# Optimization experiments

Measured on AMD Instinct MI355X. Metric: run time of the kernel, lower is better.

Reference implementation:

```python
import jax, jax.numpy as jnp
import numpy as np
import math

N, C, T, V = 32, 64, 400, 27
S = 2            # num_subset
IC = 16          # inter_channels
EPS = 1e-5


def _spatial_pe(channels, num_node):
    # PositionalEncoding(domain='spatial'): pe[c, t, v] depends only on joint id v
    pos = jnp.arange(num_node, dtype=jnp.float32)                      # [V]
    div = jnp.exp(jnp.arange(0, channels, 2, dtype=jnp.float32)
                  * (-math.log(10000.0) / channels))                   # [C/2]
    ang = div[:, None] * pos[None, :]                                  # [C/2, V]
    pe = jnp.stack([jnp.sin(ang), jnp.cos(ang)], axis=1)               # [C/2, 2, V]
    return pe.reshape(channels, num_node)                              # [C, V]


def _conv1x1(x, w, b):
    # x: [N, Cin, T, V], w: [Cout, Cin]
    return jnp.einsum('nctv,oc->notv', x, w) + b[None, :, None, None]


def _bn(x, g, b, m, v):
    inv = g / jnp.sqrt(v + EPS)
    return x * inv[None, :, None, None] + (b - m * inv)[None, :, None, None]


def _leaky(x):
    return jnp.where(x >= 0, x, 0.1 * x)


def setup_inputs() -> dict:
    key = jax.random.key(0)
    ks = jax.random.split(key, 24)
    d = {}
    d['x'] = jax.random.normal(ks[0], (N, C, T, V), jnp.float32)
    d['w_in'] = jax.random.normal(ks[1], (2 * S * IC, C), jnp.float32) * 0.1
    d['b_in'] = jax.random.normal(ks[2], (2 * S * IC,), jnp.float32) * 0.05
    d['alphas'] = jnp.ones((1, S, 1, 1), jnp.float32)
    d['att0'] = jax.random.uniform(ks[3], (1, S, V, V), jnp.float32) / V
    d['w_outs'] = jax.random.normal(ks[4], (C, S * C), jnp.float32) * 0.08
    d['b_outs'] = jax.random.normal(ks[5], (C,), jnp.float32) * 0.05
    d['bn_outs_g'] = jax.random.uniform(ks[6], (C,), jnp.float32) + 0.5
    d['bn_outs_b'] = jax.random.normal(ks[7], (C,), jnp.float32) * 0.05
    d['bn_outs_m'] = jax.random.normal(ks[8], (C,), jnp.float32) * 0.1
    d['bn_outs_v'] = jax.random.uniform(ks[9], (C,), jnp.float32) + 0.5
    d['w_ff'] = jax.random.normal(ks[10], (C, C), jnp.float32) * 0.1
    d['b_ff'] = jax.random.normal(ks[11], (C,), jnp.float32) * 0.05
    d['bn_ff_g'] = jax.random.uniform(ks[12], (C,), jnp.float32) + 0.5
    d['bn_ff_b'] = jax.random.normal(ks[13], (C,), jnp.float32) * 0.05
    d['bn_ff_m'] = jax.random.normal(ks[14], (C,), jnp.float32) * 0.1
    d['bn_ff_v'] = jax.random.uniform(ks[15], (C,), jnp.float32) + 0.5
    d['w_t'] = jax.random.normal(ks[16], (C, C, 3, 1), jnp.float32) * 0.08
    d['b_t'] = jax.random.normal(ks[17], (C,), jnp.float32) * 0.05
    d['bn_t_g'] = jax.random.uniform(ks[18], (C,), jnp.float32) + 0.5
    d['bn_t_b'] = jax.random.normal(ks[19], (C,), jnp.float32) * 0.05
    d['bn_t_m'] = jax.random.normal(ks[20], (C,), jnp.float32) * 0.1
    d['bn_t_v'] = jax.random.uniform(ks[21], (C,), jnp.float32) + 0.5
    return d


def reference(x, w_in, b_in, alphas, att0,
              w_outs, b_outs, bn_outs_g, bn_outs_b, bn_outs_m, bn_outs_v,
              w_ff, b_ff, bn_ff_g, bn_ff_b, bn_ff_m, bn_ff_v,
              w_t, b_t, bn_t_g, bn_t_b, bn_t_m, bn_t_v):
    n, c, t, v = x.shape
    # spatial positional encoding (broadcast over T)
    pe = _spatial_pe(c, v)                                      # [C, V]
    y = x + pe[None, :, None, :]
    # q/k projection: 1x1 conv -> [N, 2S, IC, T, V], chunk on subset axis
    qk = _conv1x1(y, w_in, b_in).reshape(n, 2 * S, IC, t, v)
    q, k = qk[:, :S], qk[:, S:]
    # tanh attention over joints + learnable global bias (atts buffer is zeros)
    att = jnp.tanh(jnp.einsum('nsctu,nsctv->nsuv', q, k) / (IC * t)) * alphas
    att = att + att0                                            # [N, S, V, V]
    # aggregate V-dim: [N, S, C, T, V] -> [N, S*C, T, V]
    y = jnp.einsum('nctu,nsuv->nsctv', x, att).reshape(n, S * c, t, v)
    y = _bn(_conv1x1(y, w_outs, b_outs), bn_outs_g, bn_outs_b, bn_outs_m, bn_outs_v)
    y = _leaky(x + y)                                           # downs1 = identity
    y2 = _bn(_conv1x1(y, w_ff, b_ff), bn_ff_g, bn_ff_b, bn_ff_m, bn_ff_v)
    y2 = _leaky(x + y2)                                         # downs2 = identity
    # temporal conv (3,1), padding (1,0), stride 1
    z = jax.lax.conv_general_dilated(
        y2, w_t, window_strides=(1, 1), padding=((1, 1), (0, 0)),
        dimension_numbers=('NCHW', 'OIHW', 'NCHW')) + b_t[None, :, None, None]
    z = _bn(z, bn_t_g, bn_t_b, bn_t_m, bn_t_v)
    z = _leaky(y2 + z)                                          # downt2 = identity
    return z
```

## Files before the change

### kernel.cpp

```cpp
#include <hip/hip_runtime.h>
#include <hip/hip_bf16.h>
#include <math.h>


typedef __hip_bfloat16 bf16;
typedef unsigned short u16t;
typedef unsigned int u32t;

using bf16x8 = __attribute__((ext_vector_type(8))) short;
using f32x4  = __attribute__((ext_vector_type(4))) float;

#define NN 32
#define CH 64
#define TT 400
#define VV 27
#define PIX 10800
#define NSUV (32*2*27*27)
#define XTOT (NN*CH*PIX)

#define TB1 4
#define NT1 100
#define TB2 4
#define NT2 100
#define TBS 9
#define NTS 45

__device__ __forceinline__ float lrelu(float x) { return x >= 0.f ? x : 0.1f * x; }
__device__ __forceinline__ float4 ld4(const float* p) { return *reinterpret_cast<const float4*>(p); }
__device__ __forceinline__ uint2 ld2u(const u32t* p) { return *reinterpret_cast<const uint2*>(p); }

__device__ __forceinline__ u16t f2bf(float f) {
    return __bfloat16_as_ushort(__float2bfloat16(f));
}
__device__ __forceinline__ u32t packbf(float lo, float hi) {
    return ((u32t)f2bf(hi) << 16) | (u32t)f2bf(lo);
}
__device__ __forceinline__ float bf2f(u16t u) {
    return __uint_as_float(((u32t)u) << 16);
}
__device__ __forceinline__ u32t cvtpk(float lo, float hi) {
    u32t r;
    asm("v_cvt_pk_bf16_f32 %0, %1, %2" : "=v"(r) : "v"(lo), "v"(hi));
    return r;
}
__device__ __forceinline__ void dot2v(float& c, u32t a, u32t b) {
    asm("v_dot2_f32_bf16 %0, %1, %2, %0" : "+v"(c) : "v"(a), "v"(b));
}
__device__ __forceinline__ void dot2s(float& c, u32t a_sgpr, u32t b) {
    asm("v_dot2_f32_bf16 %0, %1, %2, %0" : "+v"(c) : "s"(a_sgpr), "v"(b));
}

__global__ void k_prep(
    const float* __restrict__ w_outs, const float* __restrict__ b_outs,
    const float* __restrict__ go, const float* __restrict__ bo,
    const float* __restrict__ mo, const float* __restrict__ vo,
    const float* __restrict__ w_ff, const float* __restrict__ b_ff,
    const float* __restrict__ gf, const float* __restrict__ bf,
    const float* __restrict__ mf, const float* __restrict__ vf,
    const float* __restrict__ w_t, const float* __restrict__ b_t,
    const float* __restrict__ gt, const float* __restrict__ btb,
    const float* __restrict__ mt, const float* __restrict__ vt,
    const float* __restrict__ w_in,
    u16t* __restrict__ wfoA, float* __restrict__ bfo,
    u16t* __restrict__ wffA, float* __restrict__ bff,
    u16t* __restrict__ wtA, float* __restrict__ bft,
    u32t* __restrict__ wqkpk)
{
    const int total = 8192 + 4096 + 12288 + 192 + 2048;
    for (int idx = blockIdx.x * 256 + threadIdx.x; idx < total; idx += gridDim.x * 256) {
        if (idx < 8192) {
            int o = idx >> 7, j = idx & 127;
            float inv = go[o] * rsqrtf(vo[o] + 1e-5f);
            wfoA[idx] = f2bf(w_outs[o * 128 + j] * inv);
        } else if (idx < 12288) {
            int r = idx - 8192; int o = r >> 6, c = r & 63;
            float inv = gf[o] * rsqrtf(vf[o] + 1e-5f);
            wffA[r] = f2bf(w_ff[o * 64 + c] * inv);
        } else if (idx < 24576) {
            int r = idx - 12288;
            int o = r / 192, k2 = r % 192;
            int kt = k2 >> 6, c = k2 & 63;
            float inv = gt[o] * rsqrtf(vt[o] + 1e-5f);
            wtA[r] = f2bf(w_t[o * 192 + c * 3 + kt] * inv);
        } else if (idx < 24768) {
            int r = idx - 24576; int o = r & 63, which = r >> 6;
            if (which == 0) {
                float inv = go[o] * rsqrtf(vo[o] + 1e-5f);
                bfo[o] = b_outs[o] * inv + bo[o] - mo[o] * inv;
            } else if (which == 1) {
                float inv = gf[o] * rsqrtf(vf[o] + 1e-5f);
                bff[o] = b_ff[o] * inv + bf[o] - mf[o] * inv;
            } else {
                float inv = gt[o] * rsqrtf(vt[o] + 1e-5f);
                bft[o] = b_t[o] * inv + btb[o] - mt[o] * inv;
            }
        } else {
            int i = idx - 24768;
            int cc2 = i & 31, c = (i >> 5) & 15, sq = i >> 9;
            int s = sq >> 1, qk = sq & 1;
            int row = qk * 32 + s * 16 + c;
            wqkpk[i] = packbf(w_in[row * 64 + 2 * cc2], w_in[row * 64 + 2 * cc2 + 1]);
        }
    }
}

__global__ __launch_bounds__(256) void k_pbias(
    const float* __restrict__ w_in, const float* __restrict__ b_in,
    float* __restrict__ pb)
{
    __shared__ float pe[64 * 27];
    const int tid = threadIdx.x;
    for (int idx = tid; idx < 1728; idx += 256) {
        int c = idx / 27, u = idx % 27;
        float div = expf(-0.28782313662425575f * (float)(c >> 1));
        float ang = div * (float)u;
        pe[idx] = (c & 1) ? cosf(ang) : sinf(ang);
    }
    __syncthreads();
    for (int idx = tid; idx < 1792; idx += 256) {
        int u = idx % 28, r = idx / 28;
        int c = r % 16, sq = r / 16;
        if (u >= 27) { pb[idx] = 0.f; continue; }
        int s = sq >> 1, qk = sq & 1;
        int row = qk * 32 + s * 16 + c;
        float acc = b_in[row];
        for (int cc = 0; cc < 64; ++cc) acc += w_in[row * 64 + cc] * pe[cc * 27 + u];
        pb[idx] = acc;
    }
}

__global__ __launch_bounds__(256, 4) void k_scores(
    const float* __restrict__ x, const u32t* __restrict__ wqkpk,
    const float* __restrict__ pb, float* __restrict__ scores)
{
    const int tid = threadIdx.x;
    const int s = blockIdx.y, n = blockIdx.z;
    const int t0 = blockIdx.x * TBS;

    __shared__ u32t qlds[TBS * 27 * 10];
    __shared__ u32t klds[TBS * 27 * 10];

    const int pcl = tid < 243 ? tid : 242;
    const int tt = pcl / 27, u = pcl - tt * 27;
    const int t = t0 + tt;
    const bool valid = (tid < 243) && (t < TT);

    u32t xp[32];
    const float* xb = x + (size_t)n * 64 * PIX + (size_t)(t < TT ? t : 0) * 27 + u;
    #pragma unroll
    for (int c2 = 0; c2 < 32; ++c2) {
        float v0 = xb[(size_t)(2 * c2) * PIX];
        float v1 = xb[(size_t)(2 * c2 + 1) * PIX];
        xp[c2] = cvtpk(v0, v1);
    }

    const float* pbq = pb + ((s * 2 + 0) * 16) * 28 + u;
    const float* pbk = pb + ((s * 2 + 1) * 16) * 28 + u;
    const u32t* wq = wqkpk + (s * 2 + 0) * 16 * 32;
    const u32t* wk = wqkpk + (s * 2 + 1) * 16 * 32;
    float qr[16], kr[16];
    #pragma unroll
    for (int c = 0; c < 16; ++c) { qr[c] = pbq[c * 28]; kr[c] = pbk[c * 28]; }
    #pragma unroll
    for (int c = 0; c < 16; ++c) {
        const u32t* wr = wq + c * 32;
        #pragma unroll
        for (int c2 = 0; c2 < 32; ++c2) dot2s(qr[c], wr[c2], xp[c2]);
    }
    #pragma unroll
    for (int c = 0; c < 16; ++c) {
        const u32t* wr = wk + c * 32;
        #pragma unroll
        for (int c2 = 0; c2 < 32; ++c2) dot2s(kr[c], wr[c2], xp[c2]);
    }

    if (tid < 243) {
        #pragma unroll
        for (int c2 = 0; c2 < 8; ++c2) {
            qlds[(tt * 27 + u) * 10 + c2] = valid ? cvtpk(qr[2 * c2], qr[2 * c2 + 1]) : 0u;
            klds[(tt * 27 + u) * 10 + c2] = valid ? cvtpk(kr[2 * c2], kr[2 * c2 + 1]) : 0u;
        }
    }
    __syncthreads();

    const int sid = tid < 243 ? tid : 242;
    const int ug = sid / 9, vg = sid % 9;
    const int v0 = vg * 3;
    float sc0 = 0.f, sc1 = 0.f, sc2 = 0.f;
    for (int t2 = 0; t2 < TBS; ++t2) {
        const u32t* qrow = qlds + (t2 * 27 + ug) * 10;
        const u32t* k0 = klds + (t2 * 27 + v0) * 10;
        #pragma unroll
        for (int c4 = 0; c4 < 4; ++c4) {
            uint2 qp = ld2u(qrow + c4 * 2);
            uint2 ka = ld2u(k0 + c4 * 2);
            uint2 kb = ld2u(k0 + 10 + c4 * 2);
            uint2 kc = ld2u(k0 + 20 + c4 * 2);
            dot2v(sc0, qp.x, ka.x); dot2v(sc0, qp.y, ka.y);
            dot2v(sc1, qp.x, kb.x); dot2v(sc1, qp.y, kb.y);
            dot2v(sc2, qp.x, kc.x); dot2v(sc2, qp.y, kc.y);
        }
    }
    if (tid < 243) {
        float* sb = scores + (n * 2 + s) * 729 + ug * 27 + v0;
        atomicAdd(&sb[0], sc0);
        atomicAdd(&sb[1], sc1);
        atomicAdd(&sb[2], sc2);
    }
}

__global__ void k_att(const float* __restrict__ scores,
                      const float* __restrict__ alphas,
                      const float* __restrict__ att0,
                      u32t* __restrict__ attTp)
{
    int i = blockIdx.x * 256 + threadIdx.x;
    if (i >= NN * 2 * 32 * 16) return;
    int e = i & 15;
    int r = i >> 4;
    int v = r & 31;
    int ns = r >> 5;
    int s = ns & 1;
    if (v >= 27) { attTp[i] = 0u; return; }
    const float* sb = scores + ns * 729;
    const float* ab = att0 + s * 729;
    float al = alphas[s];
    int u0 = 2 * e, u1 = 2 * e + 1;
    float a0 = (u0 < 27) ? tanhf(sb[u0 * 27 + v] * (1.f / 6400.f)) * al + ab[u0 * 27 + v] : 0.f;
    float a1 = (u1 < 27) ? tanhf(sb[u1 * 27 + v] * (1.f / 6400.f)) * al + ab[u1 * 27 + v] : 0.f;
    attTp[i] = packbf(a0, a1);
}

__global__ __launch_bounds__(512, 4) void k_stage1(
    const float* __restrict__ x, const u32t* __restrict__ attTp,
    const u16t* __restrict__ wfoA, const float* __restrict__ bfo,
    const u16t* __restrict__ wffA, const float* __restrict__ bff,
    u16t* __restrict__ y2T)
{
    const int tid = threadIdx.x;
    const int n = blockIdx.y, t0 = blockIdx.x * TB1;
    const int w = tid >> 6, li = tid & 15, g = (tid >> 4) & 3;

    __shared__ __align__(16) u16t xs[4 * 64 * 32];
    __shared__ __align__(16) u32t mmL[112 * 68];
    __shared__ __align__(16) u32t y1L[112 * 34];

    for (int j = tid; j < 4096; j += 512) {
        int i = j & 15, c = (j >> 4) & 63, tt = j >> 10;
        const float* xrow = x + (size_t)(n * 64 + c) * PIX + (size_t)(t0 + tt) * 27;
        int u0 = 2 * i;
        float v0 = (u0 < 27) ? xrow[u0] : 0.f;
        float v1 = (u0 + 1 < 27) ? xrow[u0 + 1] : 0.f;
        int ip = i ^ (((c >> 1) & 3) << 2);
        reinterpret_cast<u32t*>(xs)[(tt * 64 + c) * 16 + ip] = packbf(v0, v1);
    }
    __syncthreads();

    {
        const int t = w & 3, s = w >> 2;
        bf16x8 ax[4];
        #pragma unroll
        for (int Mt = 0; Mt < 4; ++Mt) {
            const int c = Mt * 16 + li;
            const int blk = g ^ ((li >> 1) & 3);
            ax[Mt] = *reinterpret_cast<const bf16x8*>(&xs[(t * 64 + c) * 32 + blk * 8]);
        }
        const u16t* attp16 = reinterpret_cast<const u16t*>(attTp);
        #pragma unroll
        for (int Nt = 0; Nt < 2; ++Nt) {
            bf16x8 b = *reinterpret_cast<const bf16x8*>(
                &attp16[(((n * 2 + s) * 32) + Nt * 16 + li) * 32 + g * 8]);
            const int v = Nt * 16 + li;
            #pragma unroll
            for (int Mt = 0; Mt < 4; ++Mt) {
                f32x4 d = {0.f, 0.f, 0.f, 0.f};
                d = __builtin_amdgcn_mfma_f32_16x16x32_bf16(ax[Mt], b, d, 0, 0, 0);
                if (v < 28) {
                    const int p = t * 28 + v;
                    const int j2 = s * 32 + Mt * 8 + g * 2;
                    mmL[p * 68 + j2]     = packbf(d[0], d[1]);
                    mmL[p * 68 + j2 + 1] = packbf(d[2], d[3]);
                }
            }
        }
    }
    __syncthreads();

    const int ot = w & 3, hh = w >> 2;
    const int o0 = ot * 16 + g * 4;

    {
        bf16x8 aw[4];
        #pragma unroll
        for (int Ks = 0; Ks < 4; ++Ks)
            aw[Ks] = *reinterpret_cast<const bf16x8*>(&wfoA[(ot * 16 + li) * 128 + Ks * 32 + g * 8]);
        float4 bf4 = ld4(&bfo[o0]);
        #pragma unroll
        for (int q = 0; q < 4; ++q) {
            const int Nt = hh * 4 + q;
            if (Nt >= 7) continue;
            f32x4 d = {0.f, 0.f, 0.f, 0.f};
            #pragma unroll
            for (int Ks = 0; Ks < 4; ++Ks) {
                bf16x8 b = *reinterpret_cast<const bf16x8*>(&mmL[(Nt * 16 + li) * 68 + Ks * 16 + g * 4]);
                d = __builtin_amdgcn_mfma_f32_16x16x32_bf16(aw[Ks], b, d, 0, 0, 0);
            }
            const int p = Nt * 16 + li;
            const int tt = p / 28, v = p - tt * 28;
            const int sw0 = ((o0 >> 1) & 3) << 3;
            const int sw1 = (((o0 + 2) >> 1) & 3) << 3;
            float ya = lrelu(bf2f(xs[(tt * 64 + o0 + 0) * 32 + (v ^ sw0)]) + d[0] + bf4.x);
            float yb = lrelu(bf2f(xs[(tt * 64 + o0 + 1) * 32 + (v ^ sw0)]) + d[1] + bf4.y);
            float yc = lrelu(bf2f(xs[(tt * 64 + o0 + 2) * 32 + (v ^ sw1)]) + d[2] + bf4.z);
            float yd = lrelu(bf2f(xs[(tt * 64 + o0 + 3) * 32 + (v ^ sw1)]) + d[3] + bf4.w);
            y1L[p * 34 + ot * 8 + g * 2]     = packbf(ya, yb);
            y1L[p * 34 + ot * 8 + g * 2 + 1] = packbf(yc, yd);
        }
    }
    __syncthreads();

    {
        bf16x8 af[2];
        #pragma unroll
        for (int Ks = 0; Ks < 2; ++Ks)
            af[Ks] = *reinterpret_cast<const bf16x8*>(&wffA[(ot * 16 + li) * 64 + Ks * 32 + g * 8]);
        float4 bff4 = ld4(&bff[o0]);
        #pragma unroll
        for (int q = 0; q < 4; ++q) {
            const int Nt = hh * 4 + q;
            if (Nt >= 7) continue;
            f32x4 d = {0.f, 0.f, 0.f, 0.f};
            #pragma unroll
            for (int Ks = 0; Ks < 2; ++Ks) {
                union { uint2 u2[2]; bf16x8 v8; } bu;
                bu.u2[0] = *reinterpret_cast<const uint2*>(&y1L[(Nt * 16 + li) * 34 + Ks * 16 + g * 4]);
                bu.u2[1] = *reinterpret_cast<const uint2*>(&y1L[(Nt * 16 + li) * 34 + Ks * 16 + g * 4 + 2]);
                d = __builtin_amdgcn_mfma_f32_16x16x32_bf16(af[Ks], bu.v8, d, 0, 0, 0);
            }
            const int p = Nt * 16 + li;
            const int tt = p / 28, v = p - tt * 28;
            if (v < 27) {
                const int sw0 = ((o0 >> 1) & 3) << 3;
                const int sw1 = (((o0 + 2) >> 1) & 3) << 3;
                float r0 = lrelu(bf2f(xs[(tt * 64 + o0 + 0) * 32 + (v ^ sw0)]) + d[0] + bff4.x);
                float r1 = lrelu(bf2f(xs[(tt * 64 + o0 + 1) * 32 + (v ^ sw0)]) + d[1] + bff4.y);
                float r2 = lrelu(bf2f(xs[(tt * 64 + o0 + 2) * 32 + (v ^ sw1)]) + d[2] + bff4.z);
                float r3 = lrelu(bf2f(xs[(tt * 64 + o0 + 3) * 32 + (v ^ sw1)]) + d[3] + bff4.w);
                uint2 st;
                st.x = packbf(r0, r1);
                st.y = packbf(r2, r3);
                size_t P = (size_t)n * PIX + (size_t)(t0 + tt) * 27 + v;
                *reinterpret_cast<uint2*>(y2T + P * 64 + o0) = st;
            }
        }
    }
}

__global__ __launch_bounds__(256, 4) void k_stage2(
    const u16t* __restrict__ y2T, const u16t* __restrict__ wtA,
    const float* __restrict__ bft, float* __restrict__ out)
{
    const int tid = threadIdx.x;
    const int n = blockIdx.y, t0 = blockIdx.x * TB2;
    const int w = tid >> 6, li = tid & 15, g = (tid >> 4) & 3;

    __shared__ __align__(16) u16t ys[6 * 28 * 72];

    for (int idx = tid; idx < 6 * 27 * 8; idx += 256) {
        int q = idx & 7, r = idx >> 3;
        int v = r % 27, tp = r / 27;
        int t = t0 - 1 + tp;
        uint4 val = {0u, 0u, 0u, 0u};
        if (t >= 0 && t < TT)
            val = *reinterpret_cast<const uint4*>(
                &y2T[((size_t)n * PIX + (size_t)t * 27 + v) * 64 + q * 8]);
        *reinterpret_cast<uint4*>(&ys[(tp * 28 + v) * 72 + q * 8]) = val;
    }
    for (int idx = tid; idx < 6 * 8; idx += 256) {
        int q = idx & 7, tp = idx >> 3;
        uint4 z = {0u, 0u, 0u, 0u};
        *reinterpret_cast<uint4*>(&ys[(tp * 28 + 27) * 72 + q * 8]) = z;
    }
    __syncthreads();

    const int o0 = w * 16 + g * 4;
    bf16x8 aw[6];
    #pragma unroll
    for (int Ks = 0; Ks < 6; ++Ks)
        aw[Ks] = *reinterpret_cast<const bf16x8*>(&wtA[(w * 16 + li) * 192 + Ks * 32 + g * 8]);
    float4 bt4 = ld4(&bft[o0]);

    #pragma unroll
    for (int Nt = 0; Nt < 7; ++Nt) {
        const int p = Nt * 16 + li;
        const int tt = p / 28, v = p - tt * 28;
        f32x4 d = {0.f, 0.f, 0.f, 0.f};
        #pragma unroll
        for (int Ks = 0; Ks < 6; ++Ks) {
            const int kt = Ks >> 1, c0 = (Ks & 1) * 32 + g * 8;
            bf16x8 b = *reinterpret_cast<const bf16x8*>(&ys[((tt + kt) * 28 + v) * 72 + c0]);
            d = __builtin_amdgcn_mfma_f32_16x16x32_bf16(aw[Ks], b, d, 0, 0, 0);
        }
        if (v < 27) {
            float* ob = out + (size_t)(n * 64) * PIX + (size_t)(t0 + tt) * 27 + v;
            float r0 = bf2f(ys[((tt + 1) * 28 + v) * 72 + o0 + 0]);
            float r1 = bf2f(ys[((tt + 1) * 28 + v) * 72 + o0 + 1]);
            float r2 = bf2f(ys[((tt + 1) * 28 + v) * 72 + o0 + 2]);
            float r3 = bf2f(ys[((tt + 1) * 28 + v) * 72 + o0 + 3]);
            ob[(size_t)(o0 + 0) * PIX] = lrelu(r0 + d[0] + bt4.x);
            ob[(size_t)(o0 + 1) * PIX] = lrelu(r1 + d[1] + bt4.y);
            ob[(size_t)(o0 + 2) * PIX] = lrelu(r2 + d[2] + bt4.z);
            ob[(size_t)(o0 + 3) * PIX] = lrelu(r3 + d[3] + bt4.w);
        }
    }
}

extern "C" void kernel_launch(void* const* d_in, const int* in_sizes, int n_in,
                              void* d_out, int out_size, void* d_ws, size_t ws_size,
                              hipStream_t stream)
{
    const float* x      = (const float*)d_in[0];
    const float* w_in   = (const float*)d_in[1];
    const float* b_in   = (const float*)d_in[2];
    const float* alphas = (const float*)d_in[3];
    const float* att0   = (const float*)d_in[4];
    const float* w_outs = (const float*)d_in[5];
    const float* b_outs = (const float*)d_in[6];
    const float* bog    = (const float*)d_in[7];
    const float* bob    = (const float*)d_in[8];
    const float* bom    = (const float*)d_in[9];
    const float* bov    = (const float*)d_in[10];
    const float* w_ff   = (const float*)d_in[11];
    const float* b_ff   = (const float*)d_in[12];
    const float* bfg    = (const float*)d_in[13];
    const float* bfb    = (const float*)d_in[14];
    const float* bfm    = (const float*)d_in[15];
    const float* bfv    = (const float*)d_in[16];
    const float* w_t    = (const float*)d_in[17];
    const float* b_t    = (const float*)d_in[18];
    const float* btg    = (const float*)d_in[19];
    const float* btb    = (const float*)d_in[20];
    const float* btm    = (const float*)d_in[21];
    const float* btv    = (const float*)d_in[22];

    float* pbw    = (float*)d_ws;
    float* scores = pbw + 1792;
    u32t*  attTp  = (u32t*)(scores + NSUV);
    u16t*  wfoA   = (u16t*)(attTp + 32768);
    u16t*  wffA   = (u16t*)((u32t*)wfoA + 4096);
    u16t*  wtA    = (u16t*)((u32t*)wffA + 2048);
    float* bfo    = (float*)((u32t*)wtA + 6144);
    float* bff    = bfo + 64;
    float* bft    = bff + 64;
    u32t*  wqkpk  = (u32t*)(bft + 64);
    u16t*  y2T    = (u16t*)(wqkpk + 2048);

    hipMemsetAsync(scores, 0, NSUV * sizeof(float), stream);

    k_prep<<<32, 256, 0, stream>>>(w_outs, b_outs, bog, bob, bom, bov,
                                   w_ff, b_ff, bfg, bfb, bfm, bfv,
                                   w_t, b_t, btg, btb, btm, btv, w_in,
                                   wfoA, bfo, wffA, bff, wtA, bft, wqkpk);
    k_pbias<<<1, 256, 0, stream>>>(w_in, b_in, pbw);
    k_scores<<<dim3(NTS, 2, NN), 256, 0, stream>>>(x, wqkpk, pbw, scores);
    k_att<<<(NN * 2 * 32 * 16 + 255) / 256, 256, 0, stream>>>(scores, alphas, att0, attTp);
    k_stage1<<<dim3(NT1, NN), 512, 0, stream>>>(x, attTp, wfoA, bfo, wffA, bff, y2T);
    k_stage2<<<dim3(NT2, NN), 256, 0, stream>>>(y2T, wtA, bft, (float*)d_out);
}
```

Baseline: 355.2 us.

## Pre-transpose x to pixel-major bf16 and merge prep, pbias and memset launches

Adds a kernel that converts x into a pixel-major bf16 buffer with 64 contiguous channels per pixel. k_scores then loads each pixel's channels with 16-byte vector loads instead of 64 strided fp32 loads. The prep, positional-bias and score-zeroing work are folded into one 34-block launch, which drops two launches and a memset. The cost is an extra full pass over x (read fp32, write bf16) before k_scores, and the shared buffer is reused afterwards for y2T.

```diff
diff --git a/kernel.cpp b/kernel.cpp
--- a/kernel.cpp
+++ b/kernel.cpp
@@ -24,6 +24,8 @@
 #define NT2 100
 #define TBS 9
 #define NTS 45
+#define XP_PB 216
+#define NXT 50
 
 __device__ __forceinline__ float lrelu(float x) { return x >= 0.f ? x : 0.1f * x; }
 __device__ __forceinline__ float4 ld4(const float* p) { return *reinterpret_cast<const float4*>(p); }
@@ -50,7 +52,7 @@
     asm("v_dot2_f32_bf16 %0, %1, %2, %0" : "+v"(c) : "s"(a_sgpr), "v"(b));
 }
 
-__global__ void k_prep(
+__global__ __launch_bounds__(256) void k_prep_all(
     const float* __restrict__ w_outs, const float* __restrict__ b_outs,
     const float* __restrict__ go, const float* __restrict__ bo,
     const float* __restrict__ mo, const float* __restrict__ vo,
@@ -60,14 +62,46 @@
     const float* __restrict__ w_t, const float* __restrict__ b_t,
     const float* __restrict__ gt, const float* __restrict__ btb,
     const float* __restrict__ mt, const float* __restrict__ vt,
-    const float* __restrict__ w_in,
+    const float* __restrict__ w_in, const float* __restrict__ b_in,
     u16t* __restrict__ wfoA, float* __restrict__ bfo,
     u16t* __restrict__ wffA, float* __restrict__ bff,
     u16t* __restrict__ wtA, float* __restrict__ bft,
-    u32t* __restrict__ wqkpk)
-{
+    u32t* __restrict__ wqkpk, float* __restrict__ pbw,
+    float* __restrict__ scores)
+{
+    const int tid = threadIdx.x;
+    const int bx = blockIdx.x;
+
+    if (bx == 32) {
+        __shared__ float pe[64 * 27];
+        for (int idx = tid; idx < 1728; idx += 256) {
+            int c = idx / 27, u = idx % 27;
+            float div = expf(-0.28782313662425575f * (float)(c >> 1));
+            float ang = div * (float)u;
+            pe[idx] = (c & 1) ? cosf(ang) : sinf(ang);
+        }
+        __syncthreads();
+        for (int idx = tid; idx < 1792; idx += 256) {
+            int u = idx % 28, r = idx / 28;
+            int c = r % 16, sq = r / 16;
+            if (u >= 27) { pbw[idx] = 0.f; continue; }
+            int s = sq >> 1, qk = sq & 1;
+            int row = qk * 32 + s * 16 + c;
+            float acc = b_in[row];
+            for (int cc = 0; cc < 64; ++cc) acc += w_in[row * 64 + cc] * pe[cc * 27 + u];
+            pbw[idx] = acc;
+        }
+        return;
+    }
+    if (bx == 33) {
+        float4 z = {0.f, 0.f, 0.f, 0.f};
+        for (int idx = tid; idx < NSUV / 4; idx += 256)
+            *reinterpret_cast<float4*>(scores + idx * 4) = z;
+        return;
+    }
+
     const int total = 8192 + 4096 + 12288 + 192 + 2048;
-    for (int idx = blockIdx.x * 256 + threadIdx.x; idx < total; idx += gridDim.x * 256) {
+    for (int idx = bx * 256 + tid; idx < total; idx += 32 * 256) {
         if (idx < 8192) {
             int o = idx >> 7, j = idx & 127;
             float inv = go[o] * rsqrtf(vo[o] + 1e-5f);
@@ -104,33 +138,36 @@
     }
 }
 
-__global__ __launch_bounds__(256) void k_pbias(
-    const float* __restrict__ w_in, const float* __restrict__ b_in,
-    float* __restrict__ pb)
-{
-    __shared__ float pe[64 * 27];
+__global__ __launch_bounds__(256, 8) void k_xT(
+    const float* __restrict__ x, u16t* __restrict__ xT)
+{
     const int tid = threadIdx.x;
-    for (int idx = tid; idx < 1728; idx += 256) {
-        int c = idx / 27, u = idx % 27;
-        float div = expf(-0.28782313662425575f * (float)(c >> 1));
-        float ang = div * (float)u;
-        pe[idx] = (c & 1) ? cosf(ang) : sinf(ang);
+    const int n = blockIdx.y, p0 = blockIdx.x * XP_PB;
+
+    __shared__ u16t tile[64 * 217];
+
+    for (int idx = tid; idx < 64 * XP_PB; idx += 256) {
+        int c = idx / XP_PB, p = idx - c * XP_PB;
+        tile[c * 217 + p] = f2bf(x[(size_t)(n * 64 + c) * PIX + p0 + p]);
     }
     __syncthreads();
-    for (int idx = tid; idx < 1792; idx += 256) {
-        int u = idx % 28, r = idx / 28;
-        int c = r % 16, sq = r / 16;
-        if (u >= 27) { pb[idx] = 0.f; continue; }
-        int s = sq >> 1, qk = sq & 1;
-        int row = qk * 32 + s * 16 + c;
-        float acc = b_in[row];
-        for (int cc = 0; cc < 64; ++cc) acc += w_in[row * 64 + cc] * pe[cc * 27 + u];
-        pb[idx] = acc;
+
+    for (int idx = tid; idx < XP_PB * 8; idx += 256) {
+        int p = idx >> 3, q = idx & 7;
+        u16t v[8];
+        #pragma unroll
+        for (int k = 0; k < 8; ++k) v[k] = tile[(q * 8 + k) * 217 + p];
+        uint4 st;
+        st.x = ((u32t)v[1] << 16) | v[0];
+        st.y = ((u32t)v[3] << 16) | v[2];
+        st.z = ((u32t)v[5] << 16) | v[4];
+        st.w = ((u32t)v[7] << 16) | v[6];
+        *reinterpret_cast<uint4*>(&xT[((size_t)n * PIX + p0 + p) * 64 + q * 8]) = st;
     }
 }
 
 __global__ __launch_bounds__(256, 4) void k_scores(
-    const float* __restrict__ x, const u32t* __restrict__ wqkpk,
+    const u16t* __restrict__ xT, const u32t* __restrict__ wqkpk,
     const float* __restrict__ pb, float* __restrict__ scores)
 {
     const int tid = threadIdx.x;
@@ -146,12 +183,17 @@
     const bool valid = (tid < 243) && (t < TT);
 
     u32t xp[32];
-    const float* xb = x + (size_t)n * 64 * PIX + (size_t)(t < TT ? t : 0) * 27 + u;
-    #pragma unroll
-    for (int c2 = 0; c2 < 32; ++c2) {
-        float v0 = xb[(size_t)(2 * c2) * PIX];
-        float v1 = xb[(size_t)(2 * c2 + 1) * PIX];
-        xp[c2] = cvtpk(v0, v1);
+    {
+        const u32t* xr = reinterpret_cast<const u32t*>(
+            xT + ((size_t)n * PIX + (size_t)(t < TT ? t : 0) * 27 + u) * 64);
+        #pragma unroll
+        for (int q = 0; q < 8; ++q) {
+            uint4 vv = *reinterpret_cast<const uint4*>(xr + q * 4);
+            xp[q * 4 + 0] = vv.x;
+            xp[q * 4 + 1] = vv.y;
+            xp[q * 4 + 2] = vv.z;
+            xp[q * 4 + 3] = vv.w;
+        }
     }
 
     const float* pbq = pb + ((s * 2 + 0) * 16) * 28 + u;
@@ -453,17 +495,17 @@
     float* bff    = bfo + 64;
     float* bft    = bff + 64;
     u32t*  wqkpk  = (u32t*)(bft + 64);
-    u16t*  y2T    = (u16t*)(wqkpk + 2048);
-
-    hipMemsetAsync(scores, 0, NSUV * sizeof(float), stream);
-
-    k_prep<<<32, 256, 0, stream>>>(w_outs, b_outs, bog, bob, bom, bov,
-                                   w_ff, b_ff, bfg, bfb, bfm, bfv,
-                                   w_t, b_t, btg, btb, btm, btv, w_in,
-                                   wfoA, bfo, wffA, bff, wtA, bft, wqkpk);
-    k_pbias<<<1, 256, 0, stream>>>(w_in, b_in, pbw);
-    k_scores<<<dim3(NTS, 2, NN), 256, 0, stream>>>(x, wqkpk, pbw, scores);
+    u16t*  shbuf  = (u16t*)(wqkpk + 2048);
+
+    k_prep_all<<<34, 256, 0, stream>>>(w_outs, b_outs, bog, bob, bom, bov,
+                                       w_ff, b_ff, bfg, bfb, bfm, bfv,
+                                       w_t, b_t, btg, btb, btm, btv,
+                                       w_in, b_in,
+                                       wfoA, bfo, wffA, bff, wtA, bft,
+                                       wqkpk, pbw, scores);
+    k_xT<<<dim3(NXT, NN), 256, 0, stream>>>(x, shbuf);
+    k_scores<<<dim3(NTS, 2, NN), 256, 0, stream>>>(shbuf, wqkpk, pbw, scores);
     k_att<<<(NN * 2 * 32 * 16 + 255) / 256, 256, 0, stream>>>(scores, alphas, att0, attTp);
-    k_stage1<<<dim3(NT1, NN), 512, 0, stream>>>(x, attTp, wfoA, bfo, wffA, bff, y2T);
-    k_stage2<<<dim3(NT2, NN), 256, 0, stream>>>(y2T, wtA, bft, (float*)d_out);
-}
+    k_stage1<<<dim3(NT1, NN), 512, 0, stream>>>(x, attTp, wfoA, bfo, wffA, bff, shbuf);
+    k_stage2<<<dim3(NT2, NN), 256, 0, stream>>>(shbuf, wtA, bft, (float*)d_out);
+}
```

Result: slower. 382.8 us (+7.8%).
